# Performance work log

Measured on AMD Instinct MI355X. Metric: run time of the kernel, lower is better.

Reference implementation:

```python
import jax, jax.numpy as jnp
import numpy as np

D = 2048      # d_model
QH = 32       # query heads
KVH = 8       # kv heads
HD = D // QH  # head_dim = 64
B = 2
S = 2048
THETA = 1000000.0


def _rope_cos_sin(seq_len, hd, dtype):
    inv_freq = 1.0 / (THETA ** (jnp.arange(0, hd, 2, dtype=jnp.float32) / hd))
    t = jnp.arange(seq_len, dtype=jnp.float32)
    freqs = jnp.einsum('i,j->ij', t, inv_freq)          # [S, hd/2]
    emb = jnp.concatenate([freqs, freqs], axis=-1)      # [S, hd]
    cos = jnp.cos(emb)[None, :, None, :].astype(dtype)  # [1,S,1,hd]
    sin = jnp.sin(emb)[None, :, None, :].astype(dtype)
    return cos, sin


def _rotate_half(x):
    half = x.shape[-1] // 2
    x1, x2 = x[..., :half], x[..., half:]
    return jnp.concatenate([-x2, x1], axis=-1)


def setup_inputs() -> dict:
    key = jax.random.key(0)
    ks = jax.random.split(key, 9)
    inp = {
        'q': jax.random.normal(ks[0], (B, S, D), dtype=jnp.float32),
        'k': jax.random.normal(ks[1], (B, S, D), dtype=jnp.float32),
        'v': jax.random.normal(ks[2], (B, S, D), dtype=jnp.float32),
        'attn_mask': jnp.ones((B, S), dtype=jnp.float32),  # ignored by source math
        'Wq': jax.random.normal(ks[3], (D, D), dtype=jnp.float32) * 0.02,
        'Wk': jax.random.normal(ks[4], (D, KVH * HD), dtype=jnp.float32) * 0.02,
        'Wv': jax.random.normal(ks[5], (D, KVH * HD), dtype=jnp.float32) * 0.02,
        'Wo': jax.random.normal(ks[6], (D, D), dtype=jnp.float32) * 0.02,
        'bo': jnp.zeros((D,), dtype=jnp.float32),
    }
    return inp


def reference(q, k, v, attn_mask, Wq, Wk, Wv, Wo, bo):
    b, s, _ = q.shape
    qh = (q @ Wq).reshape(b, s, QH, HD)
    kh = (k @ Wk).reshape(b, s, KVH, HD)
    vh = (v @ Wv).reshape(b, s, KVH, HD)

    cos, sin = _rope_cos_sin(s, HD, qh.dtype)
    qh = qh * cos + _rotate_half(qh) * sin
    kh = kh * cos + _rotate_half(kh) * sin

    g = QH // KVH
    # torch .repeat tiles the head axis: [h0..h7, h0..h7, ...]
    kh = jnp.tile(kh, (1, 1, g, 1))  # [b,s,QH,HD]
    vh = jnp.tile(vh, (1, 1, g, 1))

    qt = qh.transpose(0, 2, 1, 3)  # [b,QH,s,HD]
    kt = kh.transpose(0, 2, 1, 3)
    vt = vh.transpose(0, 2, 1, 3)

    scale = 1.0 / jnp.sqrt(jnp.asarray(HD, dtype=qt.dtype))
    scores = jnp.einsum('bhqd,bhkd->bhqk', qt, kt) * scale
    # source passes attn_mask=None, is_causal=False when a mask is given:
    # full non-causal attention, mask value unused.
    attn = jax.nn.softmax(scores, axis=-1)
    out = jnp.einsum('bhqk,bhkd->bhqd', attn, vt)
    out = out.transpose(0, 2, 1, 3).reshape(b, s, D)
    return out @ Wo + bo
```

## Files before the change

kernel.cpp:

```cpp
#include <hip/hip_runtime.h>
#include <math.h>

#define D_    2048
#define QH_   32
#define KVH_  8
#define HD_   64
#define B_    2
#define S_    2048
#define NROW_ (B_*S_)
#define KVD_  (KVH_*HD_)
#define LOG2E 1.44269504f

typedef __bf16 bf16;
typedef __bf16 bf16x2 __attribute__((ext_vector_type(2)));
typedef __bf16 bf16x4 __attribute__((ext_vector_type(4)));
typedef __bf16 bf16x8 __attribute__((ext_vector_type(8)));
typedef float  f32x4  __attribute__((ext_vector_type(4)));
typedef float  f32x16 __attribute__((ext_vector_type(16)));

__device__ __forceinline__ f32x4 mfma16(bf16x8 a, bf16x8 b, f32x4 c) {
  return __builtin_amdgcn_mfma_f32_16x16x32_bf16(a, b, c, 0, 0, 0);
}
__device__ __forceinline__ f32x16 mfma32(bf16x8 a, bf16x8 b, f32x16 c) {
  return __builtin_amdgcn_mfma_f32_32x32x16_bf16(a, b, c, 0, 0, 0);
}

__device__ __forceinline__ void gload_lds16(const bf16* g, bf16* l) {
  __builtin_amdgcn_global_load_lds(
      (const __attribute__((address_space(1))) void*)g,
      (__attribute__((address_space(3))) void*)l, 16, 0, 0);
}

__device__ __forceinline__ unsigned pack_bf16(float a, float b) {
  union { bf16x2 v; unsigned u; } t;
  t.v[0] = (bf16)a; t.v[1] = (bf16)b;
  return t.u;
}

__global__ void k_ropetab(float2* __restrict__ tab) {
  int idx = blockIdx.x * 256 + threadIdx.x;
  int s = idx >> 5, d = idx & 31;
  float invf = exp2f(-(float)d * 0.62286151f);
  float ang = (float)s * invf;
  float sn, cs;
  sincosf(ang, &sn, &cs);
  tab[idx] = make_float2(cs, sn);
}

__global__ void k_convert(const float* __restrict__ in, bf16* __restrict__ out, int n4) {
  int i = blockIdx.x * 256 + threadIdx.x;
  if (i >= n4) return;
  f32x4 v = ((const f32x4*)in)[i];
  bf16x4 o;
#pragma unroll
  for (int j = 0; j < 4; j++) o[j] = (bf16)v[j];
  ((bf16x4*)out)[i] = o;
}

__device__ __forceinline__ void transpose_w_body(const float* W, bf16* Wt, int K, int N) {
  __shared__ float tile[32][33];
  int n0 = blockIdx.x * 32, k0 = blockIdx.y * 32;
  int tx = threadIdx.x, ty = threadIdx.y;
#pragma unroll
  for (int j = 0; j < 4; j++)
    tile[ty + 8*j][tx] = W[(size_t)(k0 + ty + 8*j) * N + n0 + tx];
  __syncthreads();
#pragma unroll
  for (int j = 0; j < 4; j++)
    Wt[(size_t)(n0 + ty + 8*j) * K + k0 + tx] = (bf16)tile[tx][ty + 8*j];
}

__global__ void k_transpose_w(const float* __restrict__ W, bf16* __restrict__ Wt,
                              int K, int N) {
  transpose_w_body(W, Wt, K, N);
}

__global__ void k_transpose_w2(const float* __restrict__ W0, const float* __restrict__ W1,
                               bf16* __restrict__ T0, bf16* __restrict__ T1) {
  transpose_w_body(blockIdx.z ? W1 : W0, blockIdx.z ? T1 : T0, D_, KVD_);
}

template<int EPI>
__device__ __forceinline__ void gemm_body(bf16* Asb, bf16* Bsb,
                                          const bf16* A, const bf16* Bt, void* Cout,
                                          const float* bias, const float2* tab,
                                          int M, int N, int K) {
  int tid = threadIdx.x;
  int wave = tid >> 6, lane = tid & 63, hi = lane >> 4, lr = lane & 15;
  int wm = wave >> 1, wn = wave & 1;
  int m0 = blockIdx.y * 128, n0 = blockIdx.x * 128;
  f32x4 acc[4][4] = {};
  int nk = K >> 6;

  int s_row[4], s_dch[4];
#pragma unroll
  for (int i = 0; i < 4; i++) {
    int c = i * 256 + tid;
    s_row[i] = c >> 3;
    s_dch[i] = (c & 7) ^ (s_row[i] & 7);
  }

#define GSTAGE(buf, kt_)                                                       \
  do {                                                                         \
    int k0_ = (kt_) * 64;                                                      \
    _Pragma("unroll")                                                          \
    for (int i = 0; i < 4; i++) {                                              \
      gload_lds16(A  + (size_t)(m0 + s_row[i]) * K + k0_ + s_dch[i] * 8,       \
                  Asb + ((buf) * 8192 + (i * 256 + wave * 64) * 8));           \
      gload_lds16(Bt + (size_t)(n0 + s_row[i]) * K + k0_ + s_dch[i] * 8,       \
                  Bsb + ((buf) * 8192 + (i * 256 + wave * 64) * 8));           \
    }                                                                          \
  } while (0)

  GSTAGE(0, 0);
  __syncthreads();

  for (int kt = 0; kt < nk; kt++) {
    int cur = kt & 1;
    if (kt + 1 < nk) GSTAGE(cur ^ 1, kt + 1);
#pragma unroll
    for (int kk = 0; kk < 2; kk++) {
      bf16x8 af[4], bfr[4];
#pragma unroll
      for (int mt = 0; mt < 4; mt++) {
        int row = wm * 64 + mt * 16 + lr;
        int sl = (kk * 4 + hi) ^ (row & 7);
        af[mt] = *(const bf16x8*)(Asb + cur * 8192 + row * 64 + sl * 8);
      }
#pragma unroll
      for (int nt = 0; nt < 4; nt++) {
        int row = wn * 64 + nt * 16 + lr;
        int sl = (kk * 4 + hi) ^ (row & 7);
        bfr[nt] = *(const bf16x8*)(Bsb + cur * 8192 + row * 64 + sl * 8);
      }
      __builtin_amdgcn_s_setprio(1);
#pragma unroll
      for (int mt = 0; mt < 4; mt++)
#pragma unroll
        for (int nt = 0; nt < 4; nt++)
          acc[mt][nt] = mfma16(af[mt], bfr[nt], acc[mt][nt]);
      __builtin_amdgcn_s_setprio(0);
    }
    __syncthreads();
  }
#undef GSTAGE

  if (EPI == 1) {
#pragma unroll
    for (int mt = 0; mt < 4; mt++)
#pragma unroll
      for (int r = 0; r < 4; r++) {
        int grow = m0 + wm * 64 + mt * 16 + 4 * hi + r;
        int s = grow & (S_ - 1);
#pragma unroll
        for (int nt = 0; nt < 2; nt++) {
          int gcol = n0 + wn * 64 + nt * 16 + lr;
          float2 cs = tab[s * 32 + nt * 16 + lr];
          float x1 = acc[mt][nt][r], x2 = acc[mt][nt + 2][r];
          ((bf16*)Cout)[(size_t)grow * N + gcol]      = (bf16)(x1 * cs.x - x2 * cs.y);
          ((bf16*)Cout)[(size_t)grow * N + gcol + 32] = (bf16)(x2 * cs.x + x1 * cs.y);
        }
      }
  } else {
#pragma unroll
    for (int mt = 0; mt < 4; mt++)
#pragma unroll
      for (int nt = 0; nt < 4; nt++)
#pragma unroll
        for (int r = 0; r < 4; r++) {
          int grow = m0 + wm * 64 + mt * 16 + 4 * hi + r;
          int gcol = n0 + wn * 64 + nt * 16 + lr;
          ((float*)Cout)[(size_t)grow * N + gcol] = acc[mt][nt][r] + bias[gcol];
        }
  }
}

__global__ __launch_bounds__(256) void k_gemm_q(const bf16* __restrict__ A,
                                                const bf16* __restrict__ Bt,
                                                bf16* __restrict__ C,
                                                const float2* __restrict__ tab) {
  __shared__ alignas(16) bf16 As[2][128 * 64];
  __shared__ alignas(16) bf16 Bs[2][128 * 64];
  gemm_body<1>(&As[0][0], &Bs[0][0], A, Bt, C, nullptr, tab, NROW_, D_, D_);
}

__global__ __launch_bounds__(256) void k_gemm_o(const bf16* __restrict__ A,
                                                const bf16* __restrict__ Bt,
                                                float* __restrict__ C,
                                                const float* __restrict__ bias) {
  __shared__ alignas(16) bf16 As[2][128 * 64];
  __shared__ alignas(16) bf16 Bs[2][128 * 64];
  gemm_body<2>(&As[0][0], &Bs[0][0], A, Bt, C, bias, nullptr, NROW_, D_, D_);
}

template<int EPI>
__device__ __forceinline__ void gemm_body64(bf16* Asb, bf16* Bsb,
                                            const float* Af, const bf16* Bt, void* Cout,
                                            const float2* tab) {
  const int K = D_, N = KVD_;
  int tid = threadIdx.x;
  int wave = tid >> 6, lane = tid & 63, hi = lane >> 4, lr = lane & 15;
  int m0 = blockIdx.y * 64, n0 = blockIdx.x * 128;
  int nbase = (wave >> 1) * 64 + (wave & 1) * 16;
  f32x4 acc[4][2] = {};
  const int nk = K >> 6;

  int a_row[2], a_dch[2], b_row[4], b_dch[4];
#pragma unroll
  for (int i = 0; i < 2; i++) {
    int c = i * 256 + tid;
    a_row[i] = c >> 3;
    a_dch[i] = (c & 7) ^ (a_row[i] & 7);
  }
#pragma unroll
  for (int i = 0; i < 4; i++) {
    int c = i * 256 + tid;
    b_row[i] = c >> 3;
    b_dch[i] = (c & 7) ^ (b_row[i] & 7);
  }

  f32x4 areg[2][2];

#define A_LOAD(kt_)                                                            \
  do {                                                                         \
    int k0_ = (kt_) * 64;                                                      \
    _Pragma("unroll")                                                          \
    for (int i = 0; i < 2; i++) {                                              \
      const float* p = Af + (size_t)(m0 + a_row[i]) * K + k0_ + a_dch[i] * 8;  \
      areg[i][0] = *(const f32x4*)p;                                           \
      areg[i][1] = *(const f32x4*)(p + 4);                                     \
    }                                                                          \
  } while (0)

#define A_WRITE(buf)                                                           \
  do {                                                                         \
    _Pragma("unroll")                                                          \
    for (int i = 0; i < 2; i++) {                                              \
      bf16x8 v;                                                                \
      _Pragma("unroll")                                                        \
      for (int j = 0; j < 4; j++) {                                            \
        v[j]     = (bf16)areg[i][0][j];                                        \
        v[4 + j] = (bf16)areg[i][1][j];                                        \
      }                                                                        \
      *(bf16x8*)(Asb + (buf) * 4096 + (i * 256 + tid) * 8) = v;                \
    }                                                                          \
  } while (0)

#define GSTAGE_B(buf, kt_)                                                     \
  do {                                                                         \
    int k0_ = (kt_) * 64;                                                      \
    _Pragma("unroll")                                                          \
    for (int i = 0; i < 4; i++)                                                \
      gload_lds16(Bt + (size_t)(n0 + b_row[i]) * K + k0_ + b_dch[i] * 8,       \
                  Bsb + ((buf) * 8192 + (i * 256 + wave * 64) * 8));           \
  } while (0)

  A_LOAD(0);
  GSTAGE_B(0, 0);
  A_WRITE(0);
  __syncthreads();

  for (int kt = 0; kt < nk; kt++) {
    int cur = kt & 1;
    if (kt + 1 < nk) {
      A_LOAD(kt + 1);
      GSTAGE_B(cur ^ 1, kt + 1);
    }
#pragma unroll
    for (int kk = 0; kk < 2; kk++) {
      bf16x8 af[4], bfr[2];
#pragma unroll
      for (int mt = 0; mt < 4; mt++) {
        int row = mt * 16 + lr;
        int sl = (kk * 4 + hi) ^ (row & 7);
        af[mt] = *(const bf16x8*)(Asb + cur * 4096 + row * 64 + sl * 8);
      }
#pragma unroll
      for (int nt = 0; nt < 2; nt++) {
        int row = nbase + nt * 32 + lr;
        int sl = (kk * 4 + hi) ^ (row & 7);
        bfr[nt] = *(const bf16x8*)(Bsb + cur * 8192 + row * 64 + sl * 8);
      }
      __builtin_amdgcn_s_setprio(1);
#pragma unroll
      for (int mt = 0; mt < 4; mt++)
#pragma unroll
        for (int nt = 0; nt < 2; nt++) {
          if (EPI == 3) acc[mt][nt] = mfma16(bfr[nt], af[mt], acc[mt][nt]);
          else          acc[mt][nt] = mfma16(af[mt], bfr[nt], acc[mt][nt]);
        }
      __builtin_amdgcn_s_setprio(0);
    }
    if (kt + 1 < nk) A_WRITE(cur ^ 1);
    __syncthreads();
  }
#undef A_LOAD
#undef A_WRITE
#undef GSTAGE_B

  if (EPI == 1) {
#pragma unroll
    for (int mt = 0; mt < 4; mt++)
#pragma unroll
      for (int r = 0; r < 4; r++) {
        int grow = m0 + mt * 16 + 4 * hi + r;
        int s = grow & (S_ - 1);
        int d = (wave & 1) * 16 + lr;
        int gcol = n0 + nbase + lr;
        float2 cs = tab[s * 32 + d];
        float x1 = acc[mt][0][r], x2 = acc[mt][1][r];
        ((bf16*)Cout)[(size_t)grow * N + gcol]      = (bf16)(x1 * cs.x - x2 * cs.y);
        ((bf16*)Cout)[(size_t)grow * N + gcol + 32] = (bf16)(x2 * cs.x + x1 * cs.y);
      }
  } else {
    int b = m0 >> 11;
#pragma unroll
    for (int mt = 0; mt < 4; mt++)
#pragma unroll
      for (int nt = 0; nt < 2; nt++)
#pragma unroll
        for (int r = 0; r < 4; r++) {
          int n = n0 + nbase + nt * 32 + 4 * hi + r;
          int m = m0 + mt * 16 + lr;
          ((bf16*)Cout)[((size_t)(b * KVD_ + n)) * S_ + (m & (S_ - 1))] =
              (bf16)acc[mt][nt][r];
        }
  }
}

__global__ __launch_bounds__(256) void k_gemm_kv(const float* __restrict__ kf,
                                                 const float* __restrict__ vf,
                                                 const bf16* __restrict__ B0,
                                                 const bf16* __restrict__ B1,
                                                 bf16* __restrict__ Kh,
                                                 bf16* __restrict__ Vt,
                                                 const float2* __restrict__ tab) {
  __shared__ alignas(16) bf16 As[2][64 * 64];
  __shared__ alignas(16) bf16 Bs[2][128 * 64];
  if (blockIdx.z == 0) gemm_body64<1>(&As[0][0], &Bs[0][0], kf, B0, Kh, tab);
  else                 gemm_body64<3>(&As[0][0], &Bs[0][0], vf, B1, Vt, nullptr);
}

__global__ __launch_bounds__(512, 4) void k_attn(const bf16* __restrict__ Qh,
                                                 const bf16* __restrict__ Kh,
                                                 const bf16* __restrict__ Vt,
                                                 bf16* __restrict__ ctx) {
  __shared__ alignas(16) bf16 Ks[2][64 * 64];
  __shared__ alignas(16) bf16 Vs[2][64 * 64];
  int tid = threadIdx.x;
  int wave = tid >> 6, lane = tid & 63, hi2 = lane >> 5, l31 = lane & 31;
  int qt = blockIdx.x, h = blockIdx.y, b = blockIdx.z;
  int kv = h & 7;
  int q0 = qt * 256 + wave * 32;

  bf16x8 qf[4];
  {
    const float QSC = 0.125f * LOG2E;
    const bf16* qp = Qh + (size_t)(b * S_ + q0 + l31) * D_ + h * HD_ + hi2 * 8;
#pragma unroll
    for (int df = 0; df < 4; df++) {
      bf16x8 v = *(const bf16x8*)(qp + 16 * df);
#pragma unroll
      for (int j = 0; j < 8; j++) v[j] = (bf16)((float)v[j] * QSC);
      qf[df] = v;
    }
  }

  f32x16 o0, o1, accl;
#pragma unroll
  for (int i = 0; i < 16; i++) { o0[i] = 0.f; o1[i] = 0.f; accl[i] = 0.f; }
  bf16x8 ones;
#pragma unroll
  for (int j = 0; j < 8; j++) ones[j] = (bf16)1.0f;

  const bf16* Kg = Kh + (size_t)(b * S_) * KVD_ + kv * HD_;
  const bf16* Vg = Vt + (size_t)(b * KVH_ + kv) * HD_ * S_;

  int c_row = tid >> 3, c_slot = tid & 7;
  int c_dch = c_slot ^ (c_row & 7);

#define STAGE(buf, kt_)                                                        \
  do {                                                                         \
    gload_lds16(Kg + (size_t)((kt_) * 64 + c_row) * KVD_ + c_dch * 8,          \
                &Ks[buf][tid * 8]);                                            \
    gload_lds16(Vg + (size_t)c_row * S_ + (kt_) * 64 + c_dch * 8,              \
                &Vs[buf][tid * 8]);                                            \
  } while (0)

  STAGE(0, 0);
  __syncthreads();

  const int NT = S_ / 64;
  for (int kt = 0; kt < NT; kt++) {
    int cur = kt & 1;
    if (kt + 1 < NT) STAGE(cur ^ 1, kt + 1);

    const bf16* Kb = &Ks[cur][0];
    const bf16* Vb = &Vs[cur][0];

    f32x16 s0, s1;
#pragma unroll
    for (int i = 0; i < 16; i++) { s0[i] = 0.f; s1[i] = 0.f; }
    __builtin_amdgcn_s_setprio(1);
#pragma unroll
    for (int df = 0; df < 4; df++) {
      int ch = hi2 + 2 * df;
      int sl = (ch ^ (l31 & 7)) << 3;
      bf16x8 k0 = *(const bf16x8*)(Kb + l31 * 64 + sl);
      bf16x8 k1 = *(const bf16x8*)(Kb + (l31 + 32) * 64 + sl);
      s0 = mfma32(k0, qf[df], s0);
      s1 = mfma32(k1, qf[df], s1);
    }
    __builtin_amdgcn_s_setprio(0);

#pragma unroll
    for (int i = 0; i < 16; i++) s0[i] = __builtin_amdgcn_exp2f(s0[i]);
#pragma unroll
    for (int i = 0; i < 16; i++) s1[i] = __builtin_amdgcn_exp2f(s1[i]);

    unsigned Rk[2][4][2];
#pragma unroll
    for (int m = 0; m < 4; m++)
#pragma unroll
      for (int w = 0; w < 2; w++) {
        Rk[0][m][w] = pack_bf16(s0[4*m + 2*w], s0[4*m + 2*w + 1]);
        Rk[1][m][w] = pack_bf16(s1[4*m + 2*w], s1[4*m + 2*w + 1]);
      }
#pragma unroll
    for (int kf = 0; kf < 2; kf++)
#pragma unroll
      for (int kp = 0; kp < 2; kp++)
#pragma unroll
        for (int w = 0; w < 2; w++)
          asm volatile("v_permlane32_swap_b32 %0, %1"
                       : "+v"(Rk[kf][2*kp][w]), "+v"(Rk[kf][2*kp+1][w]));
    bf16x8 pf[4];
#pragma unroll
    for (int kfr = 0; kfr < 4; kfr++) {
      int kf = kfr >> 1, k2 = (kfr & 1) * 2;
      union { unsigned d[4]; bf16x8 v; } u;
      u.d[0] = Rk[kf][k2][0];     u.d[1] = Rk[kf][k2][1];
      u.d[2] = Rk[kf][k2 + 1][0]; u.d[3] = Rk[kf][k2 + 1][1];
      pf[kfr] = u.v;
    }

    __builtin_amdgcn_s_setprio(1);
#pragma unroll
    for (int kfr = 0; kfr < 4; kfr++) {
      int ch = hi2 + 2 * kfr;
      int sl = (ch ^ (l31 & 7)) << 3;
      bf16x8 v0 = *(const bf16x8*)(Vb + l31 * 64 + sl);
      bf16x8 v1 = *(const bf16x8*)(Vb + (l31 + 32) * 64 + sl);
      o0 = mfma32(pf[kfr], v0, o0);
      o1 = mfma32(pf[kfr], v1, o1);
      accl = mfma32(pf[kfr], ones, accl);
    }
    __builtin_amdgcn_s_setprio(0);
    __syncthreads();
  }
#undef STAGE

#pragma unroll
  for (int r = 0; r < 16; r++) {
    int rowq = (r & 3) + 8 * (r >> 2) + 4 * hi2;
    float inv = 1.f / accl[r];
    size_t base = (size_t)(b * S_ + q0 + rowq) * D_ + h * HD_;
    ctx[base + l31]      = (bf16)(o0[r] * inv);
    ctx[base + l31 + 32] = (bf16)(o1[r] * inv);
  }
}

extern "C" void kernel_launch(void* const* d_in, const int* in_sizes, int n_in,
                              void* d_out, int out_size, void* d_ws, size_t ws_size,
                              hipStream_t stream) {
  const float* q  = (const float*)d_in[0];
  const float* k  = (const float*)d_in[1];
  const float* v  = (const float*)d_in[2];
  const float* Wq = (const float*)d_in[4];
  const float* Wk = (const float*)d_in[5];
  const float* Wv = (const float*)d_in[6];
  const float* Wo = (const float*)d_in[7];
  const float* bo = (const float*)d_in[8];

  char* ws = (char*)d_ws;
  bf16*   A0  = (bf16*)(ws + 0);
  bf16*   A1  = (bf16*)(ws + 16777216);
  bf16*   Wt  = (bf16*)(ws + 33554432);
  bf16*   Qh  = (bf16*)(ws + 41943040);
  bf16*   Kh  = (bf16*)(ws + 58720256);
  bf16*   Vt  = (bf16*)(ws + 62914560);
  float2* tab = (float2*)(ws + 67108864);
  bf16*   WtK = Wt;
  bf16*   WtV = (bf16*)(ws + 33554432 + 2097152);
  bf16*   ctx = A1;

  const int n4 = NROW_ * D_ / 4;

  k_ropetab<<<(S_ * 32) / 256, 256, 0, stream>>>(tab);
  k_convert<<<n4 / 256, 256, 0, stream>>>(q, A0, n4);
  k_transpose_w<<<dim3(D_/32, D_/32), dim3(32, 8), 0, stream>>>(Wq, Wt, D_, D_);
  k_gemm_q<<<dim3(D_/128, NROW_/128), 256, 0, stream>>>(A0, Wt, Qh, tab);
  k_transpose_w2<<<dim3(KVD_/32, D_/32, 2), dim3(32, 8), 0, stream>>>(Wk, Wv, WtK, WtV);
  k_gemm_kv<<<dim3(KVD_/128, NROW_/64, 2), 256, 0, stream>>>(k, v, WtK, WtV, Kh, Vt, tab);
  k_attn<<<dim3(S_/256, QH_, B_), 512, 0, stream>>>(Qh, Kh, Vt, ctx);
  k_transpose_w<<<dim3(D_/32, D_/32), dim3(32, 8), 0, stream>>>(Wo, Wt, D_, D_);
  k_gemm_o<<<dim3(D_/128, NROW_/128), 256, 0, stream>>>(ctx, Wt, (float*)d_out, bo);
}
```

Measured before the change: 244.1 us.

## Fuse fp32-to-bf16 conversion into Q GEMM and compute softmax denominator with scalar sums

Removes the separate conversion kernel for q: the Q projection GEMM now loads fp32 activations into registers, converts them to bf16 and writes them to LDS, double-buffered alongside the async B loads. This drops a full read/write pass over the 16 MB fp32 input and the bf16 staging buffer. In attention, the row sum is no longer computed with an extra MFMA against a ones vector. Instead each lane accumulates exp values in a scalar, and the total is gathered with shuffles at the end, trading MFMA work for VALU adds and register-staged A loads.

```diff
diff --git a/kernel.cpp b/kernel.cpp
--- a/kernel.cpp
+++ b/kernel.cpp
@@ -45,16 +45,6 @@
   float sn, cs;
   sincosf(ang, &sn, &cs);
   tab[idx] = make_float2(cs, sn);
-}
-
-__global__ void k_convert(const float* __restrict__ in, bf16* __restrict__ out, int n4) {
-  int i = blockIdx.x * 256 + threadIdx.x;
-  if (i >= n4) return;
-  f32x4 v = ((const f32x4*)in)[i];
-  bf16x4 o;
-#pragma unroll
-  for (int j = 0; j < 4; j++) o[j] = (bf16)v[j];
-  ((bf16x4*)out)[i] = o;
 }
 
 __device__ __forceinline__ void transpose_w_body(const float* W, bf16* Wt, int K, int N) {
@@ -145,43 +135,134 @@
   }
 #undef GSTAGE
 
-  if (EPI == 1) {
-#pragma unroll
-    for (int mt = 0; mt < 4; mt++)
+#pragma unroll
+  for (int mt = 0; mt < 4; mt++)
+#pragma unroll
+    for (int nt = 0; nt < 4; nt++)
 #pragma unroll
       for (int r = 0; r < 4; r++) {
         int grow = m0 + wm * 64 + mt * 16 + 4 * hi + r;
-        int s = grow & (S_ - 1);
-#pragma unroll
-        for (int nt = 0; nt < 2; nt++) {
-          int gcol = n0 + wn * 64 + nt * 16 + lr;
-          float2 cs = tab[s * 32 + nt * 16 + lr];
-          float x1 = acc[mt][nt][r], x2 = acc[mt][nt + 2][r];
-          ((bf16*)Cout)[(size_t)grow * N + gcol]      = (bf16)(x1 * cs.x - x2 * cs.y);
-          ((bf16*)Cout)[(size_t)grow * N + gcol + 32] = (bf16)(x2 * cs.x + x1 * cs.y);
-        }
-      }
-  } else {
-#pragma unroll
-    for (int mt = 0; mt < 4; mt++)
-#pragma unroll
-      for (int nt = 0; nt < 4; nt++)
-#pragma unroll
-        for (int r = 0; r < 4; r++) {
-          int grow = m0 + wm * 64 + mt * 16 + 4 * hi + r;
-          int gcol = n0 + wn * 64 + nt * 16 + lr;
-          ((float*)Cout)[(size_t)grow * N + gcol] = acc[mt][nt][r] + bias[gcol];
-        }
-  }
-}
-
-__global__ __launch_bounds__(256) void k_gemm_q(const bf16* __restrict__ A,
+        int gcol = n0 + wn * 64 + nt * 16 + lr;
+        ((float*)Cout)[(size_t)grow * N + gcol] = acc[mt][nt][r] + bias[gcol];
+      }
+}
+
+__global__ __launch_bounds__(256) void k_gemm_q(const float* __restrict__ Af,
                                                 const bf16* __restrict__ Bt,
                                                 bf16* __restrict__ C,
                                                 const float2* __restrict__ tab) {
   __shared__ alignas(16) bf16 As[2][128 * 64];
   __shared__ alignas(16) bf16 Bs[2][128 * 64];
-  gemm_body<1>(&As[0][0], &Bs[0][0], A, Bt, C, nullptr, tab, NROW_, D_, D_);
+  bf16* Asb = &As[0][0];
+  bf16* Bsb = &Bs[0][0];
+  const int M = NROW_, N = D_, K = D_;
+  int tid = threadIdx.x;
+  int wave = tid >> 6, lane = tid & 63, hi = lane >> 4, lr = lane & 15;
+  int wm = wave >> 1, wn = wave & 1;
+  int m0 = blockIdx.y * 128, n0 = blockIdx.x * 128;
+  f32x4 acc[4][4] = {};
+  const int nk = K >> 6;
+
+  int s_row[4], s_dch[4];
+#pragma unroll
+  for (int i = 0; i < 4; i++) {
+    int c = i * 256 + tid;
+    s_row[i] = c >> 3;
+    s_dch[i] = (c & 7) ^ (s_row[i] & 7);
+  }
+
+  f32x4 areg[4][2];
+
+#define A_LOADQ(kt_)                                                           \
+  do {                                                                         \
+    int k0_ = (kt_) * 64;                                                      \
+    _Pragma("unroll")                                                          \
+    for (int i = 0; i < 4; i++) {                                              \
+      const float* p = Af + (size_t)(m0 + s_row[i]) * K + k0_ + s_dch[i] * 8;  \
+      areg[i][0] = *(const f32x4*)p;                                           \
+      areg[i][1] = *(const f32x4*)(p + 4);                                     \
+    }                                                                          \
+  } while (0)
+
+#define A_WRITEQ(buf)                                                          \
+  do {                                                                         \
+    _Pragma("unroll")                                                          \
+    for (int i = 0; i < 4; i++) {                                              \
+      bf16x8 v;                                                                \
+      _Pragma("unroll")                                                        \
+      for (int j = 0; j < 4; j++) {                                            \
+        v[j]     = (bf16)areg[i][0][j];                                        \
+        v[4 + j] = (bf16)areg[i][1][j];                                        \
+      }                                                                        \
+      *(bf16x8*)(Asb + (buf) * 8192 + (i * 256 + tid) * 8) = v;                \
+    }                                                                          \
+  } while (0)
+
+#define GSTAGE_BQ(buf, kt_)                                                    \
+  do {                                                                         \
+    int k0_ = (kt_) * 64;                                                      \
+    _Pragma("unroll")                                                          \
+    for (int i = 0; i < 4; i++)                                                \
+      gload_lds16(Bt + (size_t)(n0 + s_row[i]) * K + k0_ + s_dch[i] * 8,       \
+                  Bsb + ((buf) * 8192 + (i * 256 + wave * 64) * 8));           \
+  } while (0)
+
+  A_LOADQ(0);
+  GSTAGE_BQ(0, 0);
+  A_WRITEQ(0);
+  __syncthreads();
+
+  for (int kt = 0; kt < nk; kt++) {
+    int cur = kt & 1;
+    if (kt + 1 < nk) {
+      A_LOADQ(kt + 1);
+      GSTAGE_BQ(cur ^ 1, kt + 1);
+    }
+#pragma unroll
+    for (int kk = 0; kk < 2; kk++) {
+      bf16x8 af[4], bfr[4];
+#pragma unroll
+      for (int mt = 0; mt < 4; mt++) {
+        int row = wm * 64 + mt * 16 + lr;
+        int sl = (kk * 4 + hi) ^ (row & 7);
+        af[mt] = *(const bf16x8*)(Asb + cur * 8192 + row * 64 + sl * 8);
+      }
+#pragma unroll
+      for (int nt = 0; nt < 4; nt++) {
+        int row = wn * 64 + nt * 16 + lr;
+        int sl = (kk * 4 + hi) ^ (row & 7);
+        bfr[nt] = *(const bf16x8*)(Bsb + cur * 8192 + row * 64 + sl * 8);
+      }
+      __builtin_amdgcn_s_setprio(1);
+#pragma unroll
+      for (int mt = 0; mt < 4; mt++)
+#pragma unroll
+        for (int nt = 0; nt < 4; nt++)
+          acc[mt][nt] = mfma16(af[mt], bfr[nt], acc[mt][nt]);
+      __builtin_amdgcn_s_setprio(0);
+    }
+    if (kt + 1 < nk) A_WRITEQ(cur ^ 1);
+    __syncthreads();
+  }
+#undef A_LOADQ
+#undef A_WRITEQ
+#undef GSTAGE_BQ
+
+#pragma unroll
+  for (int mt = 0; mt < 4; mt++)
+#pragma unroll
+    for (int r = 0; r < 4; r++) {
+      int grow = m0 + wm * 64 + mt * 16 + 4 * hi + r;
+      int s = grow & (S_ - 1);
+#pragma unroll
+      for (int nt = 0; nt < 2; nt++) {
+        int gcol = n0 + wn * 64 + nt * 16 + lr;
+        float2 cs = tab[s * 32 + nt * 16 + lr];
+        float x1 = acc[mt][nt][r], x2 = acc[mt][nt + 2][r];
+        C[(size_t)grow * N + gcol]      = (bf16)(x1 * cs.x - x2 * cs.y);
+        C[(size_t)grow * N + gcol + 32] = (bf16)(x2 * cs.x + x1 * cs.y);
+      }
+    }
 }
 
 __global__ __launch_bounds__(256) void k_gemm_o(const bf16* __restrict__ A,
@@ -366,12 +447,10 @@
     }
   }
 
-  f32x16 o0, o1, accl;
-#pragma unroll
-  for (int i = 0; i < 16; i++) { o0[i] = 0.f; o1[i] = 0.f; accl[i] = 0.f; }
-  bf16x8 ones;
-#pragma unroll
-  for (int j = 0; j < 8; j++) ones[j] = (bf16)1.0f;
+  float l_run = 0.f;
+  f32x16 o0, o1;
+#pragma unroll
+  for (int i = 0; i < 16; i++) { o0[i] = 0.f; o1[i] = 0.f; }
 
   const bf16* Kg = Kh + (size_t)(b * S_) * KVD_ + kv * HD_;
   const bf16* Vg = Vt + (size_t)(b * KVH_ + kv) * HD_ * S_;
@@ -413,10 +492,12 @@
     }
     __builtin_amdgcn_s_setprio(0);
 
-#pragma unroll
-    for (int i = 0; i < 16; i++) s0[i] = __builtin_amdgcn_exp2f(s0[i]);
-#pragma unroll
-    for (int i = 0; i < 16; i++) s1[i] = __builtin_amdgcn_exp2f(s1[i]);
+    float rs = 0.f;
+#pragma unroll
+    for (int i = 0; i < 16; i++) { s0[i] = __builtin_amdgcn_exp2f(s0[i]); rs += s0[i]; }
+#pragma unroll
+    for (int i = 0; i < 16; i++) { s1[i] = __builtin_amdgcn_exp2f(s1[i]); rs += s1[i]; }
+    l_run += rs;
 
     unsigned Rk[2][4][2];
 #pragma unroll
@@ -453,17 +534,17 @@
       bf16x8 v1 = *(const bf16x8*)(Vb + (l31 + 32) * 64 + sl);
       o0 = mfma32(pf[kfr], v0, o0);
       o1 = mfma32(pf[kfr], v1, o1);
-      accl = mfma32(pf[kfr], ones, accl);
     }
     __builtin_amdgcn_s_setprio(0);
     __syncthreads();
   }
 #undef STAGE
 
+  float l_full = l_run + __shfl_xor(l_run, 32, 64);
 #pragma unroll
   for (int r = 0; r < 16; r++) {
     int rowq = (r & 3) + 8 * (r >> 2) + 4 * hi2;
-    float inv = 1.f / accl[r];
+    float inv = 1.f / __shfl(l_full, rowq, 64);
     size_t base = (size_t)(b * S_ + q0 + rowq) * D_ + h * HD_;
     ctx[base + l31]      = (bf16)(o0[r] * inv);
     ctx[base + l31 + 32] = (bf16)(o1[r] * inv);
@@ -483,7 +564,6 @@
   const float* bo = (const float*)d_in[8];
 
   char* ws = (char*)d_ws;
-  bf16*   A0  = (bf16*)(ws + 0);
   bf16*   A1  = (bf16*)(ws + 16777216);
   bf16*   Wt  = (bf16*)(ws + 33554432);
   bf16*   Qh  = (bf16*)(ws + 41943040);
@@ -494,12 +574,9 @@
   bf16*   WtV = (bf16*)(ws + 33554432 + 2097152);
   bf16*   ctx = A1;
 
-  const int n4 = NROW_ * D_ / 4;
-
   k_ropetab<<<(S_ * 32) / 256, 256, 0, stream>>>(tab);
-  k_convert<<<n4 / 256, 256, 0, stream>>>(q, A0, n4);
   k_transpose_w<<<dim3(D_/32, D_/32), dim3(32, 8), 0, stream>>>(Wq, Wt, D_, D_);
-  k_gemm_q<<<dim3(D_/128, NROW_/128), 256, 0, stream>>>(A0, Wt, Qh, tab);
+  k_gemm_q<<<dim3(D_/128, NROW_/128), 256, 0, stream>>>(q, Wt, Qh, tab);
   k_transpose_w2<<<dim3(KVD_/32, D_/32, 2), dim3(32, 8), 0, stream>>>(Wk, Wv, WtK, WtV);
   k_gemm_kv<<<dim3(KVD_/128, NROW_/64, 2), 256, 0, stream>>>(k, v, WtK, WtV, Kh, Vt, tab);
   k_attn<<<dim3(S_/256, QH_, B_), 512, 0, stream>>>(Qh, Kh, Vt, ctx);
```

Measured after the change: 240.7 us. About the same (-1.4%).
